# Performance work log

Measured on AMD Instinct MI355X. Metric: run time of the kernel, lower is better.

## Reference

```python
import jax, jax.numpy as jnp
import numpy as np

N = 50000          # nodes
E = 800000         # directed edges (before self-loops)
F_IN = 256
HIDS = 32
HEADS = 8
N_CLASSES = 40
NEG_SLOPE = 0.2    # PyG GATConv default leaky_relu slope


def setup_inputs() -> dict:
    key = jax.random.key(0)
    ks = jax.random.split(key, 10)
    x = jax.random.normal(ks[0], (N, F_IN), dtype=jnp.float32)
    edge_index = jax.random.randint(ks[1], (2, E), 0, N, dtype=jnp.int32)
    # conv1: F_IN -> HIDS per head, HEADS heads, concat=True
    W1 = jax.random.normal(ks[2], (F_IN, HEADS * HIDS), dtype=jnp.float32) * (1.0 / np.sqrt(F_IN))
    a1_src = jax.random.normal(ks[3], (HEADS, HIDS), dtype=jnp.float32) * 0.1
    a1_dst = jax.random.normal(ks[4], (HEADS, HIDS), dtype=jnp.float32) * 0.1
    b1 = jnp.zeros((HEADS * HIDS,), dtype=jnp.float32)
    # conv2: HEADS*HIDS -> N_CLASSES, 1 head, concat=False
    W2 = jax.random.normal(ks[5], (HEADS * HIDS, N_CLASSES), dtype=jnp.float32) * (1.0 / np.sqrt(HEADS * HIDS))
    a2_src = jax.random.normal(ks[6], (1, N_CLASSES), dtype=jnp.float32) * 0.1
    a2_dst = jax.random.normal(ks[7], (1, N_CLASSES), dtype=jnp.float32) * 0.1
    b2 = jnp.zeros((N_CLASSES,), dtype=jnp.float32)
    return {"x": x, "edge_index": edge_index, "W1": W1, "a1_src": a1_src,
            "a1_dst": a1_dst, "b1": b1, "W2": W2, "a2_src": a2_src,
            "a2_dst": a2_dst, "b2": b2}


def _gat_conv(x, src, dst, W, a_src, a_dst, bias, heads, concat):
    n = x.shape[0]
    c = W.shape[1] // heads
    xw = (x @ W).reshape(n, heads, c)                       # [N,H,C]
    alpha_s = jnp.einsum('nhc,hc->nh', xw, a_src)           # [N,H]
    alpha_d = jnp.einsum('nhc,hc->nh', xw, a_dst)
    e = alpha_s[src] + alpha_d[dst]                         # [Etot,H]
    e = jnp.where(e >= 0, e, NEG_SLOPE * e)                 # leaky_relu
    # segment softmax over incoming edges of each destination node
    m = jax.ops.segment_max(e, dst, num_segments=n)         # [N,H]
    ex = jnp.exp(e - m[dst])
    denom = jax.ops.segment_sum(ex, dst, num_segments=n)    # [N,H]
    alpha = ex / denom[dst]                                 # [Etot,H]
    out = jax.ops.segment_sum(alpha[:, :, None] * xw[src], dst, num_segments=n)  # [N,H,C]
    if concat:
        out = out.reshape(n, heads * c)
    else:
        out = out.mean(axis=1)
    return out + bias


def reference(x, edge_index, W1, a1_src, a1_dst, b1, W2, a2_src, a2_dst, b2):
    n = x.shape[0]
    # add self-loops (PyG GATConv default)
    loop = jnp.arange(n, dtype=edge_index.dtype)
    src = jnp.concatenate([edge_index[0], loop])
    dst = jnp.concatenate([edge_index[1], loop])
    # dropout(p=0.6) layers are identity in eval mode
    h = _gat_conv(x, src, dst, W1, a1_src, a1_dst, b1, HEADS, True)
    h = jax.nn.elu(h)
    out = _gat_conv(h, src, dst, W2, a2_src, a2_dst, b2, 1, False)
    return out
```

## Files before the change

### kernel.cpp

```cpp
#include <hip/hip_runtime.h>
#include <hip/hip_bf16.h>

#define NNODES 50000
#define NPAD   50048
#define NEDGES 800000
#define ETOT   (NEDGES + NNODES)
#define FIN    256
#define HIDS   32
#define HEADS  8
#define NCLS   40
#define NEG    0.2f

#define SCAN_B 256
#define NSCB   ((NNODES + SCAN_B - 1) / SCAN_B)
#define NTILE1 ((NNODES + 63) / 64)

typedef __attribute__((ext_vector_type(8))) short bf16x8;
typedef __attribute__((ext_vector_type(4))) float f32x4;

__device__ __forceinline__ ushort f2bf(float f) {
  unsigned u = __float_as_uint(f);
  unsigned r = (u + 0x7fffu + ((u >> 16) & 1u)) >> 16;
  return (ushort)r;
}
__device__ __forceinline__ float bf2f(ushort u) {
  return __uint_as_float(((unsigned)u) << 16);
}
__device__ __forceinline__ float bflo(unsigned u) { return __uint_as_float(u << 16); }
__device__ __forceinline__ float bfhi(unsigned u) { return __uint_as_float(u & 0xffff0000u); }

__global__ __launch_bounds__(256) void prep_k(
    const float* __restrict__ W1, const float* __restrict__ W2,
    const float* __restrict__ a1src, const float* __restrict__ a1dst,
    const float* __restrict__ a2src, const float* __restrict__ a2dst,
    ushort* __restrict__ w1t, ushort* __restrict__ w2t,
    int* __restrict__ cnt, ushort* __restrict__ hb) {
  int b = blockIdx.x, t = threadIdx.x;
  if (b < 256) {
    int k = b, n = t;
    w1t[(size_t)n * 256 + k] = f2bf(W1[(size_t)k * 256 + n]);
  } else if (b < 272) {
    int j = b - 256, k = t;
    const float* av = (j < 8) ? (a1src + j * 32) : (a1dst + (j - 8) * 32);
    int nb = (j < 8) ? j * 32 : (j - 8) * 32;
    float s = 0.f;
#pragma unroll
    for (int c = 0; c < 32; ++c) s += W1[(size_t)k * 256 + nb + c] * av[c];
    w1t[(size_t)(256 + j) * 256 + k] = f2bf(s);
  } else if (b < 320) {
    w1t[(size_t)b * 256 + t] = 0;
  } else if (b < 384) {
    int n = b - 320, k = t;
    ushort v;
    if (n < NCLS) {
      v = f2bf(W2[(size_t)k * NCLS + n]);
    } else if (n == 40) {
      float s = 0.f;
#pragma unroll
      for (int c = 0; c < NCLS; ++c) s += W2[(size_t)k * NCLS + c] * a2src[c];
      v = f2bf(s);
    } else if (n == 41) {
      float s = 0.f;
#pragma unroll
      for (int c = 0; c < NCLS; ++c) s += W2[(size_t)k * NCLS + c] * a2dst[c];
      v = f2bf(s);
    } else {
      v = 0;
    }
    w2t[(size_t)n * 256 + k] = v;
  } else if (b < 580) {
    int i = (b - 384) * 256 + t;
    if (i < NNODES) cnt[i] = 0;
  } else {
    int r = NNODES + (b - 580);
    hb[(size_t)r * 256 + t] = 0;
  }
}

__global__ __launch_bounds__(256) void gemm1_mfma(
    const float* __restrict__ x, const ushort* __restrict__ w1t,
    ushort* __restrict__ xw1s, float* __restrict__ a1sx, float* __restrict__ a1dx) {
  __shared__ ushort As[64 * 40];
  __shared__ ushort Bs[320 * 40];
  const int tid = threadIdx.x;
  const int m0 = blockIdx.x * 64;
  const int w = tid >> 6, l = tid & 63, lr = l & 15, lq = l >> 4;
  f32x4 acc[4][5];
#pragma unroll
  for (int i = 0; i < 4; ++i)
#pragma unroll
    for (int j = 0; j < 5; ++j) acc[i][j] = (f32x4)0.f;

  for (int k0 = 0; k0 < 256; k0 += 32) {
    {
      int row = tid >> 2, kg = (tid & 3) * 8;
      int gr = m0 + row;
      bf16x8 av;
      if (gr < NNODES) {
        const float4* xp = (const float4*)(x + (size_t)gr * 256 + k0 + kg);
        float4 p0 = xp[0], p1 = xp[1];
        av[0] = (short)f2bf(p0.x); av[1] = (short)f2bf(p0.y);
        av[2] = (short)f2bf(p0.z); av[3] = (short)f2bf(p0.w);
        av[4] = (short)f2bf(p1.x); av[5] = (short)f2bf(p1.y);
        av[6] = (short)f2bf(p1.z); av[7] = (short)f2bf(p1.w);
      } else {
        av = (bf16x8)0;
      }
      *(bf16x8*)&As[row * 40 + kg] = av;
    }
#pragma unroll
    for (int p = 0; p < 5; ++p) {
      int idx = tid + p * 256;
      int n = idx >> 2, kg = (idx & 3) * 8;
      *(bf16x8*)&Bs[n * 40 + kg] = *(const bf16x8*)(w1t + (size_t)n * 256 + k0 + kg);
    }
    __syncthreads();
    bf16x8 af[4], bfr[5];
#pragma unroll
    for (int mt = 0; mt < 4; ++mt)
      af[mt] = *(const bf16x8*)&As[(mt * 16 + lr) * 40 + lq * 8];
#pragma unroll
    for (int nt = 0; nt < 5; ++nt) {
      int tile = nt * 4 + w;
      bfr[nt] = *(const bf16x8*)&Bs[(tile * 16 + lr) * 40 + lq * 8];
    }
#pragma unroll
    for (int mt = 0; mt < 4; ++mt)
#pragma unroll
      for (int nt = 0; nt < 5; ++nt)
        acc[mt][nt] = __builtin_amdgcn_mfma_f32_16x16x32_bf16(af[mt], bfr[nt], acc[mt][nt], 0, 0, 0);
    __syncthreads();
  }
#pragma unroll
  for (int mt = 0; mt < 4; ++mt)
#pragma unroll
    for (int nt = 0; nt < 5; ++nt) {
      int tile = nt * 4 + w;
      if (tile < 16) {
        int colc = tile * 16 + lr;
        int s = colc >> 5, c = colc & 31;
#pragma unroll
        for (int r = 0; r < 4; ++r) {
          int row = m0 + mt * 16 + lq * 4 + r;
          xw1s[((size_t)s * NPAD + row) * 32 + c] = f2bf(acc[mt][nt][r]);
        }
      } else if (tile == 16) {
#pragma unroll
        for (int r = 0; r < 4; ++r) {
          int row = m0 + mt * 16 + lq * 4 + r;
          if (lr < 8) a1sx[(size_t)lr * NPAD + row] = acc[mt][nt][r];
          else        a1dx[(size_t)(lr - 8) * NPAD + row] = acc[mt][nt][r];
        }
      }
    }
}

__global__ __launch_bounds__(256) void gemm2_mfma(
    const ushort* __restrict__ hb, const ushort* __restrict__ w2t,
    ushort* __restrict__ xw2b, float* __restrict__ a2s, float* __restrict__ a2d) {
  const int tid = threadIdx.x;
  const int w = tid >> 6, l = tid & 63, lr = l & 15, lq = l >> 4;
  const int row0 = blockIdx.x * 64 + w * 16;
  f32x4 acc[3];
#pragma unroll
  for (int i = 0; i < 3; ++i) acc[i] = (f32x4)0.f;
#pragma unroll
  for (int ks = 0; ks < 8; ++ks) {
    int k0 = ks * 32;
    bf16x8 af = *(const bf16x8*)(hb + (size_t)(row0 + lr) * 256 + k0 + lq * 8);
#pragma unroll
    for (int nt = 0; nt < 3; ++nt) {
      bf16x8 bfr = *(const bf16x8*)(w2t + (size_t)(nt * 16 + lr) * 256 + k0 + lq * 8);
      acc[nt] = __builtin_amdgcn_mfma_f32_16x16x32_bf16(af, bfr, acc[nt], 0, 0, 0);
    }
  }
#pragma unroll
  for (int nt = 0; nt < 3; ++nt) {
    int colc = nt * 16 + lr;
#pragma unroll
    for (int r = 0; r < 4; ++r) {
      int row = row0 + lq * 4 + r;
      if (colc < NCLS)      xw2b[(size_t)row * 40 + colc] = f2bf(acc[nt][r]);
      else if (colc == 40)  a2s[row] = acc[nt][r];
      else if (colc == 41)  a2d[row] = acc[nt][r];
    }
  }
}

__global__ __launch_bounds__(256) void hist_k(const int* __restrict__ dstA, int* __restrict__ cnt) {
  int e = blockIdx.x * 256 + threadIdx.x;
  if (e >= ETOT) return;
  int d = (e < NEDGES) ? dstA[e] : (e - NEDGES);
  atomicAdd(&cnt[d], 1);
}

__global__ __launch_bounds__(SCAN_B) void scan1_k(const int* __restrict__ deg,
                                                  int* __restrict__ row_ptr,
                                                  int* __restrict__ bsum) {
  __shared__ int sm[SCAN_B];
  int b = blockIdx.x, t = threadIdx.x;
  int idx = b * SCAN_B + t;
  int v = (idx < NNODES) ? deg[idx] : 0;
  sm[t] = v;
  __syncthreads();
#pragma unroll
  for (int off = 1; off < SCAN_B; off <<= 1) {
    int u = (t >= off) ? sm[t - off] : 0;
    __syncthreads();
    sm[t] += u;
    __syncthreads();
  }
  if (idx < NNODES) row_ptr[idx + 1] = sm[t];
  if (t == SCAN_B - 1) bsum[b] = sm[t];
}

__global__ __launch_bounds__(256) void scan2_k(int* __restrict__ bsum) {
  __shared__ int sm[256];
  int t = threadIdx.x;
  sm[t] = (t < NSCB) ? bsum[t] : 0;
  __syncthreads();
#pragma unroll
  for (int off = 1; off < 256; off <<= 1) {
    int u = (t >= off) ? sm[t - off] : 0;
    __syncthreads();
    sm[t] += u;
    __syncthreads();
  }
  if (t < NSCB) bsum[t] = (t > 0) ? sm[t - 1] : 0;
}

__global__ __launch_bounds__(SCAN_B) void scan3_k(const int* __restrict__ bsum,
                                                  int* __restrict__ row_ptr) {
  int b = blockIdx.x, t = threadIdx.x;
  int idx = b * SCAN_B + t;
  if (idx < NNODES) row_ptr[idx + 1] += bsum[b];
  if (b == 0 && t == 0) row_ptr[0] = 0;
}

__global__ __launch_bounds__(256) void scatter_k(const int* __restrict__ srcA, const int* __restrict__ dstA,
                                                 const int* __restrict__ row_ptr, int* __restrict__ cnt,
                                                 int* __restrict__ col) {
  int e = blockIdx.x * 256 + threadIdx.x;
  if (e >= ETOT) return;
  int s, d;
  if (e < NEDGES) { s = srcA[e]; d = dstA[e]; }
  else { s = d = e - NEDGES; }
  int old = atomicSub(&cnt[d], 1);
  col[row_ptr[d] + old - 1] = s;
}

__global__ __launch_bounds__(256) void agg1_k(
    const ushort* __restrict__ xw1s, const float* __restrict__ a1sx, const float* __restrict__ a1dx,
    const int* __restrict__ row_ptr, const int* __restrict__ col,
    const float* __restrict__ b1, ushort* __restrict__ hb) {
  const int b = blockIdx.x;
  const int s = b & 7;
  const int t = threadIdx.x;
  const int node = (b >> 3) * 64 + (t >> 2);
  const int q = t & 3;
  if (node >= NNODES) return;
  const ushort* xs = xw1s + (size_t)s * NPAD * 32 + q * 8;
  const float* as = a1sx + (size_t)s * NPAD;
  const float ad = a1dx[(size_t)s * NPAD + node];
  int i = row_ptr[node];
  const int end = row_ptr[node + 1];
  float den = 0.f;
  float c0 = 0.f, c1 = 0.f, c2 = 0.f, c3 = 0.f, c4 = 0.f, c5 = 0.f, c6 = 0.f, c7 = 0.f;
  for (; i + 2 <= end; i += 2) {
    int s0 = col[i], s1 = col[i + 1];
    uint4 u0 = *(const uint4*)(xs + (size_t)s0 * 32);
    uint4 u1 = *(const uint4*)(xs + (size_t)s1 * 32);
    float e0 = as[s0] + ad;
    float e1 = as[s1] + ad;
    float w0 = __expf(fmaxf(e0, 0.f) + NEG * fminf(e0, 0.f));
    float w1 = __expf(fmaxf(e1, 0.f) + NEG * fminf(e1, 0.f));
    den += w0 + w1;
    c0 += w0 * bflo(u0.x) + w1 * bflo(u1.x);
    c1 += w0 * bfhi(u0.x) + w1 * bfhi(u1.x);
    c2 += w0 * bflo(u0.y) + w1 * bflo(u1.y);
    c3 += w0 * bfhi(u0.y) + w1 * bfhi(u1.y);
    c4 += w0 * bflo(u0.z) + w1 * bflo(u1.z);
    c5 += w0 * bfhi(u0.z) + w1 * bfhi(u1.z);
    c6 += w0 * bflo(u0.w) + w1 * bflo(u1.w);
    c7 += w0 * bfhi(u0.w) + w1 * bfhi(u1.w);
  }
  if (i < end) {
    int s0 = col[i];
    uint4 u0 = *(const uint4*)(xs + (size_t)s0 * 32);
    float e0 = as[s0] + ad;
    float w0 = __expf(fmaxf(e0, 0.f) + NEG * fminf(e0, 0.f));
    den += w0;
    c0 += w0 * bflo(u0.x); c1 += w0 * bfhi(u0.x);
    c2 += w0 * bflo(u0.y); c3 += w0 * bfhi(u0.y);
    c4 += w0 * bflo(u0.z); c5 += w0 * bfhi(u0.z);
    c6 += w0 * bflo(u0.w); c7 += w0 * bfhi(u0.w);
  }
  const float inv = 1.f / den;
  const float4 bv0 = *reinterpret_cast<const float4*>(b1 + s * 32 + q * 8);
  const float4 bv1 = *reinterpret_cast<const float4*>(b1 + s * 32 + q * 8 + 4);
  float o[8];
  o[0] = c0 * inv + bv0.x; o[1] = c1 * inv + bv0.y;
  o[2] = c2 * inv + bv0.z; o[3] = c3 * inv + bv0.w;
  o[4] = c4 * inv + bv1.x; o[5] = c5 * inv + bv1.y;
  o[6] = c6 * inv + bv1.z; o[7] = c7 * inv + bv1.w;
  uint4 pk;
  unsigned r[4];
#pragma unroll
  for (int p = 0; p < 4; ++p) {
    float a = o[2 * p],     va = (a > 0.f) ? a : expm1f(a);
    float c = o[2 * p + 1], vc = (c > 0.f) ? c : expm1f(c);
    r[p] = (unsigned)f2bf(va) | ((unsigned)f2bf(vc) << 16);
  }
  pk.x = r[0]; pk.y = r[1]; pk.z = r[2]; pk.w = r[3];
  *(uint4*)(hb + (size_t)node * 256 + s * 32 + q * 8) = pk;
}

__global__ __launch_bounds__(256) void agg2_k(
    const ushort* __restrict__ xw2b, const float* __restrict__ a2s, const float* __restrict__ a2d,
    const int* __restrict__ row_ptr, const int* __restrict__ col,
    const float* __restrict__ b2, float* __restrict__ out, int n) {
  int wid = (blockIdx.x * 256 + threadIdx.x) >> 6;
  if (wid >= n) return;
  int lane = threadIdx.x & 63;
  int beg = row_ptr[wid], end = row_ptr[wid + 1];
  float ad = a2d[wid];
  float denom = 0.f, acc = 0.f;
  int i = beg;
  for (; i + 4 <= end; i += 4) {
    int s0 = col[i], s1 = col[i + 1], s2 = col[i + 2], s3 = col[i + 3];
    float e0 = a2s[s0] + ad;
    float e1 = a2s[s1] + ad;
    float e2 = a2s[s2] + ad;
    float e3 = a2s[s3] + ad;
    float w0 = __expf(fmaxf(e0, 0.f) + NEG * fminf(e0, 0.f));
    float w1 = __expf(fmaxf(e1, 0.f) + NEG * fminf(e1, 0.f));
    float w2 = __expf(fmaxf(e2, 0.f) + NEG * fminf(e2, 0.f));
    float w3 = __expf(fmaxf(e3, 0.f) + NEG * fminf(e3, 0.f));
    float x0 = 0.f, x1 = 0.f, x2 = 0.f, x3 = 0.f;
    if (lane < NCLS) {
      x0 = bf2f(xw2b[(size_t)s0 * 40 + lane]);
      x1 = bf2f(xw2b[(size_t)s1 * 40 + lane]);
      x2 = bf2f(xw2b[(size_t)s2 * 40 + lane]);
      x3 = bf2f(xw2b[(size_t)s3 * 40 + lane]);
    }
    denom += (w0 + w1) + (w2 + w3);
    acc += w0 * x0 + w1 * x1 + w2 * x2 + w3 * x3;
  }
  for (; i < end; ++i) {
    int s = col[i];
    float e = a2s[s] + ad;
    float w = __expf(fmaxf(e, 0.f) + NEG * fminf(e, 0.f));
    denom += w;
    if (lane < NCLS) acc += w * bf2f(xw2b[(size_t)s * 40 + lane]);
  }
  if (lane < NCLS) out[(size_t)wid * 40 + lane] = acc / denom + b2[lane];
}

extern "C" void kernel_launch(void* const* d_in, const int* in_sizes, int n_in,
                              void* d_out, int out_size, void* d_ws, size_t ws_size,
                              hipStream_t stream) {
  const float* x     = (const float*)d_in[0];
  const int*   ei    = (const int*)d_in[1];
  const float* W1    = (const float*)d_in[2];
  const float* a1src = (const float*)d_in[3];
  const float* a1dst = (const float*)d_in[4];
  const float* b1    = (const float*)d_in[5];
  const float* W2    = (const float*)d_in[6];
  const float* a2src = (const float*)d_in[7];
  const float* a2dst = (const float*)d_in[8];
  const float* b2    = (const float*)d_in[9];
  float* out = (float*)d_out;

  const int* srcA = ei;
  const int* dstA = ei + NEDGES;

  ushort* w1t  = (ushort*)d_ws;
  ushort* w2t  = w1t + (size_t)320 * 256;
  ushort* xw1s = w2t + (size_t)64 * 256;
  ushort* hb   = xw1s + (size_t)NPAD * 256;
  ushort* xw2b = hb + (size_t)NPAD * 256;
  float* a1sx  = (float*)(xw2b + (size_t)NPAD * 40);
  float* a1dx  = a1sx + (size_t)8 * NPAD;
  float* a2s   = a1dx + (size_t)8 * NPAD;
  float* a2d   = a2s + NPAD;
  int* row_ptr = (int*)(a2d + NPAD);
  int* cnt     = row_ptr + (NNODES + 1);
  int* col     = cnt + NNODES;
  int* bsum    = col + ETOT;

  prep_k<<<628, 256, 0, stream>>>(W1, W2, a1src, a1dst, a2src, a2dst, w1t, w2t, cnt, hb);

  gemm1_mfma<<<NPAD / 64, 256, 0, stream>>>(x, w1t, xw1s, a1sx, a1dx);

  hist_k<<<(ETOT + 255) / 256, 256, 0, stream>>>(dstA, cnt);
  scan1_k<<<NSCB, SCAN_B, 0, stream>>>(cnt, row_ptr, bsum);
  scan2_k<<<1, 256, 0, stream>>>(bsum);
  scan3_k<<<NSCB, SCAN_B, 0, stream>>>(bsum, row_ptr);
  scatter_k<<<(ETOT + 255) / 256, 256, 0, stream>>>(srcA, dstA, row_ptr, cnt, col);

  agg1_k<<<NTILE1 * 8, 256, 0, stream>>>(xw1s, a1sx, a1dx, row_ptr, col, b1, hb);

  gemm2_mfma<<<NPAD / 64, 256, 0, stream>>>(hb, w2t, xw2b, a2s, a2d);

  agg2_k<<<(NNODES + 3) / 4, 256, 0, stream>>>(xw2b, a2s, a2d, row_ptr, col, b2, out, NNODES);
}
```

Measured before the change: 261.3 us.

## Precompute per-edge attention weights in a separate kernel before layer-1 aggregation

Adds an ew_k kernel that computes exp(leaky_relu(a_src+a_dst)) for all 8 heads per CSR edge and stores it head-major. The scatter kernel now also records each edge's destination. The a1 score layout becomes node-major so one edge can read all heads with float4 loads. agg1_k then reads the precomputed weights instead of gathering a_src and computing exp 4 times per edge per head (once per lane quad), and is unrolled by 4. The cost is an extra launch, the extra edst array, and roughly 27 MB of extra weight traffic.

Result: no change. 263.8 us (+1.0%).

```diff
diff --git a/kernel.cpp b/kernel.cpp
--- a/kernel.cpp
+++ b/kernel.cpp
@@ -79,7 +79,7 @@
 
 __global__ __launch_bounds__(256) void gemm1_mfma(
     const float* __restrict__ x, const ushort* __restrict__ w1t,
-    ushort* __restrict__ xw1s, float* __restrict__ a1sx, float* __restrict__ a1dx) {
+    ushort* __restrict__ xw1s, float* __restrict__ a1s, float* __restrict__ a1d) {
   __shared__ ushort As[64 * 40];
   __shared__ ushort Bs[320 * 40];
   const int tid = threadIdx.x;
@@ -148,8 +148,8 @@
 #pragma unroll
         for (int r = 0; r < 4; ++r) {
           int row = m0 + mt * 16 + lq * 4 + r;
-          if (lr < 8) a1sx[(size_t)lr * NPAD + row] = acc[mt][nt][r];
-          else        a1dx[(size_t)(lr - 8) * NPAD + row] = acc[mt][nt][r];
+          if (lr < 8) a1s[(size_t)row * 8 + lr] = acc[mt][nt][r];
+          else        a1d[(size_t)row * 8 + (lr - 8)] = acc[mt][nt][r];
         }
       }
     }
@@ -239,18 +239,41 @@
 
 __global__ __launch_bounds__(256) void scatter_k(const int* __restrict__ srcA, const int* __restrict__ dstA,
                                                  const int* __restrict__ row_ptr, int* __restrict__ cnt,
-                                                 int* __restrict__ col) {
+                                                 int* __restrict__ col, int* __restrict__ edst) {
   int e = blockIdx.x * 256 + threadIdx.x;
   if (e >= ETOT) return;
   int s, d;
   if (e < NEDGES) { s = srcA[e]; d = dstA[e]; }
   else { s = d = e - NEDGES; }
   int old = atomicSub(&cnt[d], 1);
-  col[row_ptr[d] + old - 1] = s;
+  int pos = row_ptr[d] + old - 1;
+  col[pos] = s;
+  edst[pos] = d;
+}
+
+__global__ __launch_bounds__(256) void ew_k(
+    const float* __restrict__ a1s, const float* __restrict__ a1d,
+    const int* __restrict__ col, const int* __restrict__ edst,
+    float* __restrict__ ew) {
+  int pos = blockIdx.x * 256 + threadIdx.x;
+  if (pos >= ETOT) return;
+  int src = col[pos], dst = edst[pos];
+  const float4* sp = (const float4*)(a1s + (size_t)src * 8);
+  const float4* dp = (const float4*)(a1d + (size_t)dst * 8);
+  float4 s0 = sp[0], s1 = sp[1];
+  float4 d0 = dp[0], d1 = dp[1];
+  float e[8] = {s0.x + d0.x, s0.y + d0.y, s0.z + d0.z, s0.w + d0.w,
+                s1.x + d1.x, s1.y + d1.y, s1.z + d1.z, s1.w + d1.w};
+#pragma unroll
+  for (int h = 0; h < 8; ++h) {
+    float v = e[h];
+    v = fmaxf(v, 0.f) + NEG * fminf(v, 0.f);
+    ew[(size_t)h * ETOT + pos] = __expf(v);
+  }
 }
 
 __global__ __launch_bounds__(256) void agg1_k(
-    const ushort* __restrict__ xw1s, const float* __restrict__ a1sx, const float* __restrict__ a1dx,
+    const ushort* __restrict__ xw1s, const float* __restrict__ ew,
     const int* __restrict__ row_ptr, const int* __restrict__ col,
     const float* __restrict__ b1, ushort* __restrict__ hb) {
   const int b = blockIdx.x;
@@ -260,35 +283,32 @@
   const int q = t & 3;
   if (node >= NNODES) return;
   const ushort* xs = xw1s + (size_t)s * NPAD * 32 + q * 8;
-  const float* as = a1sx + (size_t)s * NPAD;
-  const float ad = a1dx[(size_t)s * NPAD + node];
+  const float* ws = ew + (size_t)s * ETOT;
   int i = row_ptr[node];
   const int end = row_ptr[node + 1];
   float den = 0.f;
   float c0 = 0.f, c1 = 0.f, c2 = 0.f, c3 = 0.f, c4 = 0.f, c5 = 0.f, c6 = 0.f, c7 = 0.f;
-  for (; i + 2 <= end; i += 2) {
-    int s0 = col[i], s1 = col[i + 1];
+  for (; i + 4 <= end; i += 4) {
+    int s0 = col[i], s1 = col[i + 1], s2 = col[i + 2], s3 = col[i + 3];
+    float w0 = ws[i], w1 = ws[i + 1], w2 = ws[i + 2], w3 = ws[i + 3];
     uint4 u0 = *(const uint4*)(xs + (size_t)s0 * 32);
     uint4 u1 = *(const uint4*)(xs + (size_t)s1 * 32);
-    float e0 = as[s0] + ad;
-    float e1 = as[s1] + ad;
-    float w0 = __expf(fmaxf(e0, 0.f) + NEG * fminf(e0, 0.f));
-    float w1 = __expf(fmaxf(e1, 0.f) + NEG * fminf(e1, 0.f));
-    den += w0 + w1;
-    c0 += w0 * bflo(u0.x) + w1 * bflo(u1.x);
-    c1 += w0 * bfhi(u0.x) + w1 * bfhi(u1.x);
-    c2 += w0 * bflo(u0.y) + w1 * bflo(u1.y);
-    c3 += w0 * bfhi(u0.y) + w1 * bfhi(u1.y);
-    c4 += w0 * bflo(u0.z) + w1 * bflo(u1.z);
-    c5 += w0 * bfhi(u0.z) + w1 * bfhi(u1.z);
-    c6 += w0 * bflo(u0.w) + w1 * bflo(u1.w);
-    c7 += w0 * bfhi(u0.w) + w1 * bfhi(u1.w);
-  }
-  if (i < end) {
+    uint4 u2 = *(const uint4*)(xs + (size_t)s2 * 32);
+    uint4 u3 = *(const uint4*)(xs + (size_t)s3 * 32);
+    den += (w0 + w1) + (w2 + w3);
+    c0 += w0 * bflo(u0.x) + w1 * bflo(u1.x) + w2 * bflo(u2.x) + w3 * bflo(u3.x);
+    c1 += w0 * bfhi(u0.x) + w1 * bfhi(u1.x) + w2 * bfhi(u2.x) + w3 * bfhi(u3.x);
+    c2 += w0 * bflo(u0.y) + w1 * bflo(u1.y) + w2 * bflo(u2.y) + w3 * bflo(u3.y);
+    c3 += w0 * bfhi(u0.y) + w1 * bfhi(u1.y) + w2 * bfhi(u2.y) + w3 * bfhi(u3.y);
+    c4 += w0 * bflo(u0.z) + w1 * bflo(u1.z) + w2 * bflo(u2.z) + w3 * bflo(u3.z);
+    c5 += w0 * bfhi(u0.z) + w1 * bfhi(u1.z) + w2 * bfhi(u2.z) + w3 * bfhi(u3.z);
+    c6 += w0 * bflo(u0.w) + w1 * bflo(u1.w) + w2 * bflo(u2.w) + w3 * bflo(u3.w);
+    c7 += w0 * bfhi(u0.w) + w1 * bfhi(u1.w) + w2 * bfhi(u2.w) + w3 * bfhi(u3.w);
+  }
+  for (; i < end; ++i) {
     int s0 = col[i];
+    float w0 = ws[i];
     uint4 u0 = *(const uint4*)(xs + (size_t)s0 * 32);
-    float e0 = as[s0] + ad;
-    float w0 = __expf(fmaxf(e0, 0.f) + NEG * fminf(e0, 0.f));
     den += w0;
     c0 += w0 * bflo(u0.x); c1 += w0 * bfhi(u0.x);
     c2 += w0 * bflo(u0.y); c3 += w0 * bfhi(u0.y);
@@ -379,26 +399,30 @@
   ushort* xw1s = w2t + (size_t)64 * 256;
   ushort* hb   = xw1s + (size_t)NPAD * 256;
   ushort* xw2b = hb + (size_t)NPAD * 256;
-  float* a1sx  = (float*)(xw2b + (size_t)NPAD * 40);
-  float* a1dx  = a1sx + (size_t)8 * NPAD;
-  float* a2s   = a1dx + (size_t)8 * NPAD;
+  float* a1s   = (float*)(xw2b + (size_t)NPAD * 40);
+  float* a1d   = a1s + (size_t)NPAD * 8;
+  float* a2s   = a1d + (size_t)NPAD * 8;
   float* a2d   = a2s + NPAD;
-  int* row_ptr = (int*)(a2d + NPAD);
+  float* ew    = a2d + NPAD;
+  int* row_ptr = (int*)(ew + (size_t)8 * ETOT);
   int* cnt     = row_ptr + (NNODES + 1);
   int* col     = cnt + NNODES;
-  int* bsum    = col + ETOT;
+  int* edst    = col + ETOT;
+  int* bsum    = edst + ETOT;
 
   prep_k<<<628, 256, 0, stream>>>(W1, W2, a1src, a1dst, a2src, a2dst, w1t, w2t, cnt, hb);
 
-  gemm1_mfma<<<NPAD / 64, 256, 0, stream>>>(x, w1t, xw1s, a1sx, a1dx);
+  gemm1_mfma<<<NPAD / 64, 256, 0, stream>>>(x, w1t, xw1s, a1s, a1d);
 
   hist_k<<<(ETOT + 255) / 256, 256, 0, stream>>>(dstA, cnt);
   scan1_k<<<NSCB, SCAN_B, 0, stream>>>(cnt, row_ptr, bsum);
   scan2_k<<<1, 256, 0, stream>>>(bsum);
   scan3_k<<<NSCB, SCAN_B, 0, stream>>>(bsum, row_ptr);
-  scatter_k<<<(ETOT + 255) / 256, 256, 0, stream>>>(srcA, dstA, row_ptr, cnt, col);
-
-  agg1_k<<<NTILE1 * 8, 256, 0, stream>>>(xw1s, a1sx, a1dx, row_ptr, col, b1, hb);
+  scatter_k<<<(ETOT + 255) / 256, 256, 0, stream>>>(srcA, dstA, row_ptr, cnt, col, edst);
+
+  ew_k<<<(ETOT + 255) / 256, 256, 0, stream>>>(a1s, a1d, col, edst, ew);
+
+  agg1_k<<<NTILE1 * 8, 256, 0, stream>>>(xw1s, ew, row_ptr, col, b1, hb);
 
   gemm2_mfma<<<NPAD / 64, 256, 0, stream>>>(hb, w2t, xw2b, a2s, a2d);
 
```
